# Performance work log

Hardware: AMD Instinct MI355X
Metric: run time of the kernel (lower is better)

Reference implementation:

```python
import jax, jax.numpy as jnp
import numpy as np

B, S, D_MODEL, H, BLOCK = 2, 4096, 1024, 16, 512
HEAD = D_MODEL // H  # 64


def setup_inputs() -> dict:
    key = jax.random.key(0)
    ks = jax.random.split(key, 5)
    w_scale = 1.0 / np.sqrt(D_MODEL)  # variance_scaling(1.0,'fan_in','normal')-like magnitude
    return {
        "inputs_q": jax.random.normal(ks[0], (B, S, D_MODEL), jnp.float32),
        "Wq": jax.random.normal(ks[1], (D_MODEL, D_MODEL), jnp.float32) * w_scale,
        "bq": jnp.zeros((D_MODEL,), jnp.float32),
        "Wk": jax.random.normal(ks[2], (D_MODEL, D_MODEL), jnp.float32) * w_scale,
        "bk": jnp.zeros((D_MODEL,), jnp.float32),
        "Wv": jax.random.normal(ks[3], (D_MODEL, D_MODEL), jnp.float32) * w_scale,
        "bv": jnp.zeros((D_MODEL,), jnp.float32),
        "Wo": jax.random.normal(ks[4], (D_MODEL, D_MODEL), jnp.float32) * w_scale,
        "bo": jnp.zeros((D_MODEL,), jnp.float32),
    }


def _flash_attention(q, k, v):
    """Blocked online-softmax attention. q,k,v: [B,S,H,D] -> [B,S,H,D].

    Scans over KV blocks of size BLOCK, maintaining running max (m),
    running sum of exp (l), and unnormalized output (o), exactly matching
    the original module's blocked accumulation math (no mask/bias/dropout).
    """
    scale = 1.0 / jnp.sqrt(jnp.asarray(HEAD, q.dtype))
    n_kv_blocks = S // BLOCK
    # [n_blocks, B, BLOCK, H, D]
    kb = k.reshape(B, n_kv_blocks, BLOCK, H, HEAD).transpose(1, 0, 2, 3, 4)
    vb = v.reshape(B, n_kv_blocks, BLOCK, H, HEAD).transpose(1, 0, 2, 3, 4)

    o0 = jnp.zeros_like(q)                                   # [B,S,H,D]
    m0 = jnp.full((B, S, H), -jnp.inf, dtype=q.dtype)        # running max
    l0 = jnp.zeros((B, S, H), dtype=q.dtype)                 # running sum-exp

    def step(carry, kv):
        o, m, l = carry
        k_blk, v_blk = kv
        # [B,H,S,BLOCK] scores for all queries vs this kv block
        scores = jnp.einsum('bqhd,bkhd->bhqk', q, k_blk) * scale
        blk_max = jnp.max(scores, axis=-1).transpose(0, 2, 1)   # [B,S,H]
        new_m = jnp.maximum(m, blk_max)
        alpha = jnp.exp(m - new_m)                               # rescale old stats
        p = jnp.exp(scores - new_m.transpose(0, 2, 1)[..., None])
        new_l = alpha * l + jnp.sum(p, axis=-1).transpose(0, 2, 1)
        new_o = o * alpha[..., None] + jnp.einsum('bhqk,bkhd->bqhd', p, v_blk)
        return (new_o, new_m, new_l), None

    (o, m, l), _ = jax.lax.scan(step, (o0, m0, l0), (kb, vb))
    return o / l[..., None]


def reference(inputs_q, Wq, bq, Wk, bk, Wv, bv, Wo, bo):
    q = (inputs_q @ Wq + bq).reshape(B, S, H, HEAD)
    k = (inputs_q @ Wk + bk).reshape(B, S, H, HEAD)  # self-attention: k=v=q input
    v = (inputs_q @ Wv + bv).reshape(B, S, H, HEAD)
    x = _flash_attention(q, k, v).reshape(B, S, D_MODEL)
    return x @ Wo + bo
```

## Files before the change

kernel.cpp:

```cpp
#include <hip/hip_runtime.h>
#include <hip/hip_bf16.h>
#include <stdint.h>

#define B_ 2
#define S_ 4096
#define DM 1024
#define H_ 16
#define HD 64
#define M_TOT (B_*S_)

typedef unsigned short u16;
typedef short s16x8 __attribute__((ext_vector_type(8)));
typedef short s16x4 __attribute__((ext_vector_type(4)));
typedef float f32x4 __attribute__((ext_vector_type(4)));
typedef uint32_t u32x2 __attribute__((ext_vector_type(2)));

#if __has_builtin(__builtin_amdgcn_mfma_f32_16x16x16_bf16)
#define MFMA16(A,B,C) __builtin_amdgcn_mfma_f32_16x16x16_bf16(A,B,C,0,0,0)
#elif __has_builtin(__builtin_amdgcn_mfma_f32_16x16x16bf16_1k)
#define MFMA16(A,B,C) __builtin_amdgcn_mfma_f32_16x16x16bf16_1k(A,B,C,0,0,0)
#else
static __device__ __forceinline__ f32x4 mfma16_asm(s16x4 a, s16x4 b, f32x4 c){
  f32x4 d;
  asm volatile("v_mfma_f32_16x16x16_bf16 %0, %1, %2, %3" : "=v"(d) : "v"(a), "v"(b), "v"(c));
  return d;
}
#define MFMA16(A,B,C) mfma16_asm(A,B,C)
#endif

__device__ __forceinline__ u16 f2bf(float f){
  union { float fv; uint32_t u; } x; x.fv = f;
  uint32_t r = (x.u + 0x7fffu + ((x.u >> 16) & 1u)) >> 16;
  return (u16)r;
}

#if __has_builtin(__builtin_amdgcn_cvt_pk_bf16_f32)
typedef __bf16 bf16x2_t __attribute__((ext_vector_type(2)));
__device__ __forceinline__ uint32_t pkbf(float a, float b){
  union { bf16x2_t v; uint32_t u; } x;
  x.v = __builtin_amdgcn_cvt_pk_bf16_f32(a, b);
  return x.u;
}
#else
__device__ __forceinline__ uint32_t pkbf(float a, float b){
  union { float f; uint32_t u; } xa, xb; xa.f = a; xb.f = b;
  return __builtin_amdgcn_perm(xb.u + 0x8000u, xa.u + 0x8000u, 0x07060302u);
}
#endif

__device__ __forceinline__ void gld_lds16(const void* g, void* l){
  __builtin_amdgcn_global_load_lds((const __attribute__((address_space(1))) void*)g,
                                   (__attribute__((address_space(3))) void*)l, 16, 0, 0);
}

__global__ __launch_bounds__(256) void k_cvt_x(const float* __restrict__ x, u16* __restrict__ xb){
  size_t i = (size_t)blockIdx.x * 256 + threadIdx.x;
  const float4* p = (const float4*)x + i*2;
  float4 a = p[0], b = p[1];
  union { u16 u[8]; uint4 v; } o;
  o.u[0]=f2bf(a.x); o.u[1]=f2bf(a.y); o.u[2]=f2bf(a.z); o.u[3]=f2bf(a.w);
  o.u[4]=f2bf(b.x); o.u[5]=f2bf(b.y); o.u[6]=f2bf(b.z); o.u[7]=f2bf(b.w);
  ((uint4*)xb)[i] = o.v;
}

__global__ __launch_bounds__(256) void k_wt(const float* __restrict__ W0, const float* __restrict__ W1,
                                            const float* __restrict__ W2, const float* __restrict__ W3,
                                            u16* __restrict__ wt){
  const float* W = blockIdx.z==0?W0: blockIdx.z==1?W1: blockIdx.z==2?W2:W3;
  u16* out = wt + (size_t)blockIdx.z * DM * DM;
  int n0 = blockIdx.x*64, k0 = blockIdx.y*64;
  __shared__ u16 T[64*66];
  int t = threadIdx.x;
  #pragma unroll
  for (int i=0;i<4;i++){
    int idx = t + i*256;
    int kr = idx >> 4, n4 = idx & 15;
    float4 v = *(const float4*)(W + (size_t)(k0+kr)*DM + n0 + n4*4);
    T[(n4*4+0)*66 + kr] = f2bf(v.x);
    T[(n4*4+1)*66 + kr] = f2bf(v.y);
    T[(n4*4+2)*66 + kr] = f2bf(v.z);
    T[(n4*4+3)*66 + kr] = f2bf(v.w);
  }
  __syncthreads();
  #pragma unroll
  for (int i=0;i<2;i++){
    int idx = t + i*256;
    int n = idx >> 3, k8 = idx & 7;
    union { u16 u[8]; uint4 v; } o;
    #pragma unroll
    for (int j=0;j<8;j++) o.u[j] = T[n*66 + k8*8 + j];
    *(uint4*)(out + (size_t)(n0+n)*DM + k0 + k8*8) = o.v;
  }
}

__device__ __forceinline__ void gemm128(const u16* __restrict__ A, const u16* __restrict__ BT,
                                        const float* __restrict__ bias, float scale,
                                        u16* __restrict__ outb, float* __restrict__ outf,
                                        int m0, int n0){
  __shared__ __align__(16) u16 As[128*32];
  __shared__ __align__(16) u16 Bs[128*32];
  int t = threadIdx.x;
  int lane = t & 63, w = t >> 6;
  int wm = w & 1, wn = w >> 1;
  int c16 = lane & 15, quad = lane >> 4;
  f32x4 acc[4][4] = {};
  for (int k0 = 0; k0 < DM; k0 += 32){
    #pragma unroll
    for (int i=0;i<2;i++){
      int idx = t + i*256;
      int row = idx >> 2, c8 = (idx & 3) << 3;
      gld_lds16(A  + (size_t)(m0+row)*DM + k0 + c8, &As[idx*8]);
      gld_lds16(BT + (size_t)(n0+row)*DM + k0 + c8, &Bs[idx*8]);
    }
    __syncthreads();
    s16x8 af[4], bf[4];
    #pragma unroll
    for (int mi=0;mi<4;mi++) af[mi] = *(const s16x8*)&As[(wm*64+mi*16+c16)*32 + quad*8];
    #pragma unroll
    for (int ni=0;ni<4;ni++) bf[ni] = *(const s16x8*)&Bs[(wn*64+ni*16+c16)*32 + quad*8];
    #pragma unroll
    for (int mi=0;mi<4;mi++)
      #pragma unroll
      for (int ni=0;ni<4;ni++)
        acc[mi][ni] = __builtin_amdgcn_mfma_f32_16x16x32_bf16(af[mi], bf[ni], acc[mi][ni], 0, 0, 0);
    __syncthreads();
  }
  #pragma unroll
  for (int mi=0;mi<4;mi++){
    #pragma unroll
    for (int ni=0;ni<4;ni++){
      int col = n0 + wn*64 + ni*16 + c16;
      float bc = bias[col];
      #pragma unroll
      for (int r=0;r<4;r++){
        int row = m0 + wm*64 + mi*16 + quad*4 + r;
        float v = (acc[mi][ni][r] + bc) * scale;
        if (outb) outb[(size_t)row*DM + col] = f2bf(v);
        else      outf[(size_t)row*DM + col] = v;
      }
    }
  }
}

#define CL2 0.18033688011112042f

__global__ __launch_bounds__(256) void k_gemm_qkv(const u16* __restrict__ xb, const u16* __restrict__ wt,
                                                  const float* __restrict__ b0, const float* __restrict__ b1,
                                                  const float* __restrict__ b2,
                                                  u16* __restrict__ q, u16* __restrict__ k, u16* __restrict__ v){
  int z = blockIdx.z;
  const u16* BT = wt + (size_t)z*DM*DM;
  const float* bias = z==0?b0: z==1?b1:b2;
  u16* out = z==0?q: z==1?k:v;
  float scale = (z==0) ? CL2 : 1.0f;
  gemm128(xb, BT, bias, scale, out, nullptr, blockIdx.y*128, blockIdx.x*128);
}

__global__ __launch_bounds__(256) void k_gemm_out(const u16* __restrict__ ab, const u16* __restrict__ wto,
                                                  const float* __restrict__ bias, float* __restrict__ out){
  gemm128(ab, wto, bias, 1.0f, nullptr, out, blockIdx.y*128, blockIdx.x*128);
}

__global__ __launch_bounds__(256) void k_vt(const u16* __restrict__ vb, u16* __restrict__ vt){
  __shared__ u16 T[64*66];
  int s0 = blockIdx.x*64, h = blockIdx.y, b = blockIdx.z;
  int t = threadIdx.x;
  #pragma unroll
  for (int i=0;i<2;i++){
    int idx = t + i*256;
    int sr = idx >> 3, d8 = idx & 7;
    s16x8 v = *(const s16x8*)(vb + ((size_t)(b*S_ + s0 + sr))*DM + h*64 + d8*8);
    #pragma unroll
    for (int j=0;j<8;j++) T[(d8*8+j)*66 + sr] = ((const u16*)&v)[j];
  }
  __syncthreads();
  #pragma unroll
  for (int i=0;i<2;i++){
    int idx = t + i*256;
    int d = idx >> 3, s8 = idx & 7;
    union { u16 u[8]; uint4 v; } o;
    #pragma unroll
    for (int j=0;j<8;j++) o.u[j] = T[d*66 + s8*8 + j];
    *(uint4*)(vt + ((size_t)((b*H_ + h)*64 + d))*S_ + s0 + s8*8) = o.v;
  }
}

__global__ __launch_bounds__(512, 2) void k_attn(const u16* __restrict__ qg, const u16* __restrict__ kg,
                                                 const u16* __restrict__ vtg, u16* __restrict__ ao){
  __shared__ __align__(16) char smem[67584];
  float* Ob  = (float*)smem;
  u16*   ObT = (u16*)smem;
  float* Lb  = (float*)(smem + 65536);

  int t = threadIdx.x, lane = t & 63, w = t >> 6;
  int c16 = lane & 15, quad = lane >> 4;
  int qq = w & 3, kh = w >> 2;
  int h = blockIdx.y, b = blockIdx.z;
  int q0 = blockIdx.x * 256;
  size_t rowbase = (size_t)b * S_;
  const u16* vbase = vtg + ((size_t)(b*H_ + h)) * 64 * S_;

  int krow0 = t >> 3,         ksw0 = ((t & 7) ^ (krow0 & 7));
  int krow1 = (t + 512) >> 3, ksw1 = ((t & 7) ^ (krow1 & 7));
  const u16* kgp0 = kg + (rowbase + krow0)*DM + h*64 + ksw0*8;
  const u16* kgp1 = kg + (rowbase + krow1)*DM + h*64 + ksw1*8;
  int vrow0 = t >> 4,         vsw0 = ((t & 15) ^ (vrow0 & 15));
  int vrow1 = (t + 512) >> 4, vsw1 = ((t & 15) ^ (vrow1 & 15));
  const u16* vgp0 = vbase + (size_t)vrow0*S_ + vsw0*8;
  const u16* vgp1 = vbase + (size_t)vrow1*S_ + vsw1*8;
  char* kd0 = smem + t*16;
  char* kd1 = smem + t*16 + 8192;
  char* vd0 = smem + 16384 + t*16;
  char* vd1 = smem + 16384 + t*16 + 8192;

  auto stage = [&](int boff, int kv0){
    size_t ko = (size_t)kv0 * DM;
    gld_lds16(kgp0 + ko, kd0 + boff);
    gld_lds16(kgp1 + ko, kd1 + boff);
    gld_lds16(vgp0 + kv0, vd0 + boff);
    gld_lds16(vgp1 + kv0, vd1 + boff);
  };

  stage(0, 0);

  s16x8 qf[4][2];
  #pragma unroll
  for (int nt=0;nt<4;nt++)
    #pragma unroll
    for (int ks=0;ks<2;ks++)
      qf[nt][ks] = *(const s16x8*)(qg + (rowbase + q0 + qq*64 + nt*16 + c16)*DM + h*64 + ks*32 + quad*8);

  f32x4 oacc[4][4] = {};
  float lacc[4] = {0.f,0.f,0.f,0.f};

  auto compute = [&](int boff){
    const u16* Kt = (const u16*)(smem + boff);
    const u16* Vt = (const u16*)(smem + boff + 16384);

    f32x4 sc[4][4] = {};
    #pragma unroll
    for (int mt=0;mt<4;mt++){
      #pragma unroll
      for (int ks=0;ks<2;ks++){
        s16x8 kf = *(const s16x8*)&Kt[(kh*64 + mt*16 + c16)*64 + (((ks*4 + quad) ^ (c16 & 7)) * 8)];
        #pragma unroll
        for (int nt=0;nt<4;nt++)
          sc[mt][nt] = __builtin_amdgcn_mfma_f32_16x16x32_bf16(kf, qf[nt][ks], sc[mt][nt], 0,0,0);
      }
    }

    uint32_t pk[4][4][2];
    #pragma unroll
    for (int mt=0;mt<4;mt++){
      #pragma unroll
      for (int nt=0;nt<4;nt++){
        float p0 = __builtin_amdgcn_exp2f(sc[mt][nt][0]);
        float p1 = __builtin_amdgcn_exp2f(sc[mt][nt][1]);
        float p2 = __builtin_amdgcn_exp2f(sc[mt][nt][2]);
        float p3 = __builtin_amdgcn_exp2f(sc[mt][nt][3]);
        lacc[nt] += (p0 + p1) + (p2 + p3);
        pk[mt][nt][0] = pkbf(p0, p1);
        pk[mt][nt][1] = pkbf(p2, p3);
      }
    }

    #pragma unroll
    for (int mt=0;mt<4;mt++){
      #pragma unroll
      for (int dt=0;dt<4;dt++){
        s16x4 vf = *(const s16x4*)&Vt[(dt*16 + c16)*128 + (((kh*8 + mt*2 + (quad>>1)) ^ c16) * 8) + (quad & 1)*4];
        #pragma unroll
        for (int nt=0;nt<4;nt++){
          union { uint32_t u[2]; s16x4 v; } pp;
          pp.u[0] = pk[mt][nt][0]; pp.u[1] = pk[mt][nt][1];
          oacc[dt][nt] = MFMA16(vf, pp.v, oacc[dt][nt]);
        }
      }
    }
  };

  #define NT (S_/128)
  #pragma unroll 1
  for (int kvt = 0; kvt < NT-1; ++kvt){
    stage(((kvt+1) & 1) * 32768, (kvt+1)*128);
    asm volatile("s_waitcnt vmcnt(4)" ::: "memory");
    __builtin_amdgcn_s_barrier();
    __builtin_amdgcn_sched_barrier(0);
    compute((kvt & 1) * 32768);
    __builtin_amdgcn_s_barrier();
    __builtin_amdgcn_sched_barrier(0);
  }
  asm volatile("s_waitcnt vmcnt(0)" ::: "memory");
  __builtin_amdgcn_s_barrier();
  __builtin_amdgcn_sched_barrier(0);
  compute(((NT-1) & 1) * 32768);

  float lw[4];
  #pragma unroll
  for (int nt=0;nt<4;nt++){
    float l = lacc[nt];
    l += __shfl_xor(l, 16);
    l += __shfl_xor(l, 32);
    lw[nt] = l;
  }
  __syncthreads();
  if (quad == 0){
    #pragma unroll
    for (int nt=0;nt<4;nt++) Lb[kh*256 + qq*64 + nt*16 + c16] = lw[nt];
  }
  uint32_t pko[4][4][2];
  float invl[4];
  #pragma unroll
  for (int dh=0; dh<2; dh++){
    if (kh == 1){
      #pragma unroll
      for (int dt2=0;dt2<2;dt2++)
        #pragma unroll
        for (int nt=0;nt<4;nt++)
          *(f32x4*)&Ob[(qq*64 + nt*16 + c16)*36 + dt2*16 + quad*4] = oacc[dh*2+dt2][nt];
    }
    __syncthreads();
    if (kh == 0){
      if (dh == 0){
        #pragma unroll
        for (int nt=0;nt<4;nt++){
          int ql = qq*64 + nt*16 + c16;
          invl[nt] = 1.0f / (Lb[ql] + Lb[256 + ql]);
        }
      }
      #pragma unroll
      for (int dt2=0;dt2<2;dt2++)
        #pragma unroll
        for (int nt=0;nt<4;nt++){
          f32x4 p = *(const f32x4*)&Ob[(qq*64 + nt*16 + c16)*36 + dt2*16 + quad*4];
          f32x4 o = oacc[dh*2+dt2][nt] + p;
          pko[dh*2+dt2][nt][0] = pkbf(o[0]*invl[nt], o[1]*invl[nt]);
          pko[dh*2+dt2][nt][1] = pkbf(o[2]*invl[nt], o[3]*invl[nt]);
        }
    }
    __syncthreads();
  }
  if (kh == 0){
    #pragma unroll
    for (int dt=0;dt<4;dt++)
      #pragma unroll
      for (int nt=0;nt<4;nt++){
        u32x2 pr; pr.x = pko[dt][nt][0]; pr.y = pko[dt][nt][1];
        *(u32x2*)&ObT[(qq*64 + nt*16 + c16)*72 + dt*16 + quad*4] = pr;
      }
  }
  __syncthreads();
  #pragma unroll
  for (int i=0;i<4;i++){
    int idx = t + i*512;
    int qr = idx >> 3, qc = (idx & 7)*8;
    *(s16x8*)(ao + (rowbase + q0 + qr)*DM + h*64 + qc) = *(const s16x8*)&ObT[qr*72 + qc];
  }
}

extern "C" void kernel_launch(void* const* d_in, const int* in_sizes, int n_in,
                              void* d_out, int out_size, void* d_ws, size_t ws_size,
                              hipStream_t stream){
  const float* x  = (const float*)d_in[0];
  const float* Wq = (const float*)d_in[1];
  const float* bq = (const float*)d_in[2];
  const float* Wk = (const float*)d_in[3];
  const float* bk = (const float*)d_in[4];
  const float* Wv = (const float*)d_in[5];
  const float* bv = (const float*)d_in[6];
  const float* Wo = (const float*)d_in[7];
  const float* bo = (const float*)d_in[8];

  char* ws = (char*)d_ws;
  const size_t XB = (size_t)M_TOT*DM*2;
  const size_t WTB = (size_t)4*DM*DM*2;
  u16* xb  = (u16*)(ws);
  u16* wt  = (u16*)(ws + XB);
  u16* qb  = (u16*)(ws + XB + WTB);
  u16* kb  = (u16*)(ws + XB + WTB + XB);
  u16* vb  = (u16*)(ws + XB + WTB + 2*XB);
  u16* vtb = (u16*)(ws + XB + WTB + 3*XB);
  u16* aob = (u16*)(ws + XB + WTB + 4*XB);

  k_cvt_x<<<dim3((M_TOT*DM)/(256*8)), 256, 0, stream>>>(x, xb);
  k_wt<<<dim3(16,16,4), 256, 0, stream>>>(Wq, Wk, Wv, Wo, wt);
  k_gemm_qkv<<<dim3(8, M_TOT/128, 3), 256, 0, stream>>>(xb, wt, bq, bk, bv, qb, kb, vb);
  k_vt<<<dim3(S_/64, H_, B_), 256, 0, stream>>>(vb, vtb);
  k_attn<<<dim3(S_/256, H_, B_), 512, 0, stream>>>(qb, kb, vtb, aob);
  k_gemm_out<<<dim3(8, M_TOT/128), 256, 0, stream>>>(aob, wt + (size_t)3*DM*DM, bo, (float*)d_out);
}
```

Baseline: 355.7 us.

## Double-buffer GEMM LDS tiles and raise wave priority around attention MFMA phases

```diff
diff --git a/kernel.cpp b/kernel.cpp
--- a/kernel.cpp
+++ b/kernel.cpp
@@ -97,34 +97,53 @@
                                         const float* __restrict__ bias, float scale,
                                         u16* __restrict__ outb, float* __restrict__ outf,
                                         int m0, int n0){
-  __shared__ __align__(16) u16 As[128*32];
-  __shared__ __align__(16) u16 Bs[128*32];
+  __shared__ __align__(16) u16 As[2][512*8];
+  __shared__ __align__(16) u16 Bs[2][512*8];
   int t = threadIdx.x;
   int lane = t & 63, w = t >> 6;
   int wm = w & 1, wn = w >> 1;
   int c16 = lane & 15, quad = lane >> 4;
+  const u16* ag0 = A  + (size_t)(m0 + (t>>2))*DM + ((t&3)<<3);
+  const u16* ag1 = A  + (size_t)(m0 + 64 + (t>>2))*DM + ((t&3)<<3);
+  const u16* bg0 = BT + (size_t)(n0 + (t>>2))*DM + ((t&3)<<3);
+  const u16* bg1 = BT + (size_t)(n0 + 64 + (t>>2))*DM + ((t&3)<<3);
   f32x4 acc[4][4] = {};
-  for (int k0 = 0; k0 < DM; k0 += 32){
-    #pragma unroll
-    for (int i=0;i<2;i++){
-      int idx = t + i*256;
-      int row = idx >> 2, c8 = (idx & 3) << 3;
-      gld_lds16(A  + (size_t)(m0+row)*DM + k0 + c8, &As[idx*8]);
-      gld_lds16(BT + (size_t)(n0+row)*DM + k0 + c8, &Bs[idx*8]);
-    }
-    __syncthreads();
+
+  auto stage = [&](int buf, int k0){
+    gld_lds16(ag0 + k0, &As[buf][t*8]);
+    gld_lds16(ag1 + k0, &As[buf][(t+256)*8]);
+    gld_lds16(bg0 + k0, &Bs[buf][t*8]);
+    gld_lds16(bg1 + k0, &Bs[buf][(t+256)*8]);
+  };
+  auto compute = [&](int buf){
     s16x8 af[4], bf[4];
     #pragma unroll
-    for (int mi=0;mi<4;mi++) af[mi] = *(const s16x8*)&As[(wm*64+mi*16+c16)*32 + quad*8];
-    #pragma unroll
-    for (int ni=0;ni<4;ni++) bf[ni] = *(const s16x8*)&Bs[(wn*64+ni*16+c16)*32 + quad*8];
+    for (int mi=0;mi<4;mi++) af[mi] = *(const s16x8*)&As[buf][(wm*64+mi*16+c16)*32 + quad*8];
+    #pragma unroll
+    for (int ni=0;ni<4;ni++) bf[ni] = *(const s16x8*)&Bs[buf][(wn*64+ni*16+c16)*32 + quad*8];
     #pragma unroll
     for (int mi=0;mi<4;mi++)
       #pragma unroll
       for (int ni=0;ni<4;ni++)
         acc[mi][ni] = __builtin_amdgcn_mfma_f32_16x16x32_bf16(af[mi], bf[ni], acc[mi][ni], 0, 0, 0);
-    __syncthreads();
-  }
+  };
+
+  stage(0, 0);
+  #pragma unroll 1
+  for (int k = 0; k < (DM/32)-1; ++k){
+    stage((k+1)&1, (k+1)*32);
+    asm volatile("s_waitcnt vmcnt(4)" ::: "memory");
+    __builtin_amdgcn_s_barrier();
+    __builtin_amdgcn_sched_barrier(0);
+    compute(k&1);
+    __builtin_amdgcn_s_barrier();
+    __builtin_amdgcn_sched_barrier(0);
+  }
+  asm volatile("s_waitcnt vmcnt(0)" ::: "memory");
+  __builtin_amdgcn_s_barrier();
+  __builtin_amdgcn_sched_barrier(0);
+  compute((DM/32-1)&1);
+
   #pragma unroll
   for (int mi=0;mi<4;mi++){
     #pragma unroll
@@ -238,6 +257,7 @@
     const u16* Vt = (const u16*)(smem + boff + 16384);
 
     f32x4 sc[4][4] = {};
+    __builtin_amdgcn_s_setprio(1);
     #pragma unroll
     for (int mt=0;mt<4;mt++){
       #pragma unroll
@@ -248,6 +268,7 @@
           sc[mt][nt] = __builtin_amdgcn_mfma_f32_16x16x32_bf16(kf, qf[nt][ks], sc[mt][nt], 0,0,0);
       }
     }
+    __builtin_amdgcn_s_setprio(0);
 
     uint32_t pk[4][4][2];
     #pragma unroll
@@ -264,6 +285,7 @@
       }
     }
 
+    __builtin_amdgcn_s_setprio(1);
     #pragma unroll
     for (int mt=0;mt<4;mt++){
       #pragma unroll
@@ -277,6 +299,7 @@
         }
       }
     }
+    __builtin_amdgcn_s_setprio(0);
   };
 
   #define NT (S_/128)
```

Result: slower. 391.2 us (+10.0%).
